# Optimization experiments

Hardware: AMD Instinct MI355X
Metric: run time of the kernel (lower is better)

The kernel has to match this reference:

```python
import jax, jax.numpy as jnp
import numpy as np

B, S, D = 4, 1024, 384
NUM_ITEMS = 16384
NUM_CLUSTERS = 256
MAX_CLUSTER_SIZE = 128  # 16384/256 = 64 real members, padded to 128 with -1
NEG_INF = -1e9


def setup_inputs() -> dict:
    key = jax.random.key(0)
    k1, k2, k3, k4, k5 = jax.random.split(key, 5)
    hidden_states = jax.random.normal(k1, (B, S, D), dtype=jnp.float32)
    item_embeddings = jax.random.normal(k2, (NUM_ITEMS, D), dtype=jnp.float32) * 0.02
    cluster_embeddings = jax.random.normal(k3, (NUM_CLUSTERS, D), dtype=jnp.float32) * 0.02
    targets = jax.random.randint(k4, (B, S), 0, NUM_ITEMS, dtype=jnp.int32)
    item_mask = (jax.random.uniform(k5, (B, S)) < 0.8).astype(jnp.float32)
    # Deterministic round-robin clustering: item i -> cluster i % C, slot i // C
    cluster_assignments = (jnp.arange(NUM_ITEMS, dtype=jnp.int32) % NUM_CLUSTERS)
    ids = (jnp.arange(NUM_CLUSTERS, dtype=jnp.int32)[:, None]
           + NUM_CLUSTERS * jnp.arange(MAX_CLUSTER_SIZE, dtype=jnp.int32)[None, :])
    cluster_indices = jnp.where(ids < NUM_ITEMS, ids, -1)  # [C, M], padded with -1
    in_cluster_id = (jnp.arange(NUM_ITEMS, dtype=jnp.int32) // NUM_CLUSTERS)
    return {
        "hidden_states": hidden_states,
        "item_embeddings": item_embeddings,
        "cluster_embeddings": cluster_embeddings,
        "item_mask": item_mask,
        "targets": targets,
        "cluster_assignments": cluster_assignments,
        "cluster_indices": cluster_indices,
        "in_cluster_id": in_cluster_id,
    }


def reference(hidden_states, item_embeddings, cluster_embeddings, item_mask,
              targets, cluster_assignments, cluster_indices, in_cluster_id):
    # Level 1: cluster logits / log-probs
    cluster_logits = jnp.einsum('bsd,cd->bsc', hidden_states, cluster_embeddings)
    cluster_log_probs = jax.nn.log_softmax(cluster_logits, axis=-1)
    target_cluster_ids = cluster_assignments[targets]                      # [B,S]
    target_cluster_log_prob = jnp.take_along_axis(
        cluster_log_probs, target_cluster_ids[..., None].astype(jnp.int32), axis=-1
    ).squeeze(-1)                                                          # [B,S]

    # Level 2: gather member embeddings of the target cluster, masked softmax
    cluster_members = cluster_indices[target_cluster_ids]                  # [B,S,M]
    member_emb = item_embeddings[jnp.maximum(cluster_members, 0)]          # [B,S,M,D]
    member_logits = jnp.einsum('bsd,bsmd->bsm', hidden_states, member_emb)  # [B,S,M]
    masked_logits = jnp.where(cluster_members != -1, member_logits, NEG_INF)
    member_log_probs = jax.nn.log_softmax(masked_logits, axis=-1)
    target_pos = in_cluster_id[targets]                                    # [B,S]
    target_item_log_prob = jnp.take_along_axis(
        member_log_probs, target_pos[..., None].astype(jnp.int32), axis=-1
    ).squeeze(-1)

    # Combined loss
    loss_per_token = -(target_cluster_log_prob + target_item_log_prob)
    total_loss = jnp.sum(loss_per_token * item_mask) / (jnp.sum(item_mask) + 1e-8)

    cluster_preds = jnp.argmax(cluster_logits, axis=-1)
    cluster_acc = jnp.mean((cluster_preds == target_cluster_ids).astype(jnp.float32))

    dummy_logits = jnp.zeros(hidden_states.shape[:2] + (item_embeddings.shape[0],),
                             dtype=hidden_states.dtype)
    return (dummy_logits, total_loss,
            -jnp.mean(target_cluster_log_prob),
            -jnp.mean(target_item_log_prob),
            cluster_acc)
```

## Files before the change

### kernel.cpp

```cpp
#include <hip/hip_runtime.h>
#include <math.h>

#define Ddim 384
#define D4 96
#define NUM_ITEMS 16384
#define NUM_CLUSTERS 256
#define MCS 128
#define NEG_INF_F (-1e9f)
#define NTOK 4096
#define TPB 16
#define NCB (NTOK / TPB)
#define NFB 512

__device__ __forceinline__ float dot4(const float4& a, const float4& b) {
    return a.x * b.x + a.y * b.y + a.z * b.z + a.w * b.w;
}

__global__ __launch_bounds__(512, 2) void hs_fused(
    const float* __restrict__ hidden,
    const float* __restrict__ item_emb,
    const float* __restrict__ cluster_emb,
    const float* __restrict__ item_mask,
    const int*   __restrict__ targets,
    const int*   __restrict__ cluster_assign,
    const int*   __restrict__ cluster_idx,
    const int*   __restrict__ in_cluster_id,
    float* __restrict__ dummy_out,
    float* __restrict__ ws)
{
    const int bid = blockIdx.x;
    const int tid = threadIdx.x;

    if (bid % 3 != 2) {
        const int fid = (bid / 3) * 2 + (bid % 3);
        float4 z; z.x = z.y = z.z = z.w = 0.f;
        float4* o4 = reinterpret_cast<float4*>(dummy_out)
                     + (size_t)fid * 512 + tid;
        #pragma unroll 8
        for (int i = 0; i < 64; ++i)
            o4[(size_t)i * (NFB * 512)] = z;
        return;
    }

    const int cb    = bid / 3;
    const int t0    = cb * TPB;
    const int lane  = tid & 63;
    const int wave  = tid >> 6;
    const int whalf = wave >> 2;
    const int wq    = wave & 3;
    const int q     = lane >> 4;
    const int r     = lane & 15;

    __shared__ float clog[TPB][NUM_CLUSTERS];
    __shared__ float mlog[TPB][64];

    const int tw = t0 + wq * 4;
    const float4* h4 = reinterpret_cast<const float4*>(hidden);
    float4 hf[4][6];
    #pragma unroll
    for (int j = 0; j < 4; ++j)
        #pragma unroll
        for (int i = 0; i < 6; ++i)
            hf[j][i] = h4[(size_t)(tw + j) * D4 + i * 16 + r];

    const float4* ce4 = reinterpret_cast<const float4*>(cluster_emb);
    #pragma unroll 2
    for (int it = 0; it < 32; ++it) {
        const int c = whalf * 128 + it * 4 + q;
        float4 ce[6];
        #pragma unroll
        for (int i = 0; i < 6; ++i) ce[i] = ce4[(size_t)c * D4 + i * 16 + r];
        float a0 = 0.f, a1 = 0.f, a2 = 0.f, a3 = 0.f;
        #pragma unroll
        for (int i = 0; i < 6; ++i) {
            a0 += dot4(ce[i], hf[0][i]);
            a1 += dot4(ce[i], hf[1][i]);
            a2 += dot4(ce[i], hf[2][i]);
            a3 += dot4(ce[i], hf[3][i]);
        }
        const bool hi8 = (r & 8) != 0;
        float u  = hi8 ? a1 : a0;
        float uS = hi8 ? a0 : a1;
        u += __shfl_xor(uS, 8);
        float w  = hi8 ? a3 : a2;
        float wS = hi8 ? a2 : a3;
        w += __shfl_xor(wS, 8);
        const bool hi4 = (r & 4) != 0;
        float zv = hi4 ? w : u;
        float zS = hi4 ? u : w;
        zv += __shfl_xor(zS, 4);
        zv += __shfl_xor(zv, 2);
        zv += __shfl_xor(zv, 1);
        if ((r & 3) == 0) {
            const int m = (r >> 2) & 3;
            const int tokj = (m == 1) ? 2 : (m == 2) ? 1 : m;
            clog[wq * 4 + tokj][c] = zv;
        }
    }
    __syncthreads();

    const int r8 = lane & 7;
    const int g8 = lane >> 3;
    const float4* ie4 = reinterpret_cast<const float4*>(item_emb);

    #pragma unroll
    for (int p = 0; p < 2; ++p) {
        const int t  = wave * 2 + p;
        const int gt = t0 + t;
        const int tgt  = targets[gt];
        const int tc   = cluster_assign[tgt];
        const int tpos = in_cluster_id[tgt];
        const float msk = item_mask[gt];

        const float v0 = clog[t][lane];
        const float v1 = clog[t][lane + 64];
        const float v2 = clog[t][lane + 128];
        const float v3 = clog[t][lane + 192];
        float bv = v0; int bi = lane;
        if (v1 > bv) { bv = v1; bi = lane + 64;  }
        if (v2 > bv) { bv = v2; bi = lane + 128; }
        if (v3 > bv) { bv = v3; bi = lane + 192; }
        #pragma unroll
        for (int m = 32; m > 0; m >>= 1) {
            const float ov = __shfl_xor(bv, m);
            const int   oi = __shfl_xor(bi, m);
            if (ov > bv || (ov == bv && oi < bi)) { bv = ov; bi = oi; }
        }
        float e = expf(v0 - bv) + expf(v1 - bv) + expf(v2 - bv) + expf(v3 - bv);
        #pragma unroll
        for (int m = 32; m > 0; m >>= 1) e += __shfl_xor(e, m);
        const float lse = bv + logf(e);
        const float tlpc = clog[t][tc] - lse;

        float4 hme[12];
        #pragma unroll
        for (int i = 0; i < 12; ++i)
            hme[i] = h4[(size_t)gt * D4 + i * 8 + r8];
        const int* crow = cluster_idx + (size_t)tc * MCS;
        #pragma unroll 2
        for (int it = 0; it < 8; ++it) {
            const int id = crow[it * 8 + g8];
            const float4* ir = ie4 + (size_t)id * D4;
            float pa = 0.f;
            #pragma unroll
            for (int i = 0; i < 12; ++i) pa += dot4(ir[i * 8 + r8], hme[i]);
            pa += __shfl_xor(pa, 1);
            pa += __shfl_xor(pa, 2);
            pa += __shfl_xor(pa, 4);
            if (r8 == 0) mlog[t][it * 8 + g8] = pa;
        }
        const float w0 = mlog[t][lane];
        float mx = w0;
        #pragma unroll
        for (int m = 32; m > 0; m >>= 1) mx = fmaxf(mx, __shfl_xor(mx, m));
        float e2 = expf(w0 - mx);
        #pragma unroll
        for (int m = 32; m > 0; m >>= 1) e2 += __shfl_xor(e2, m);
        const float tlpi = mlog[t][tpos] - (mx + logf(e2));

        if (lane == 0) {
            ws[NTOK + gt]     = msk;
            ws[2 * NTOK + gt] = tlpc;
            ws[3 * NTOK + gt] = tlpi;
            ws[4 * NTOK + gt] = (bi == tc) ? 1.f : 0.f;
        }
    }
}

__global__ __launch_bounds__(1024) void hs_final(
    const float* __restrict__ ws, float* __restrict__ out)
{
    __shared__ double red[5][1024];
    const int tid = threadIdx.x;
    double a0 = 0, a1 = 0, a2 = 0, a3 = 0, a4 = 0;
    for (int i = tid; i < NTOK; i += 1024) {
        const float msk  = ws[NTOK + i];
        const float tlpc = ws[2 * NTOK + i];
        const float tlpi = ws[3 * NTOK + i];
        a0 += (double)(-(tlpc + tlpi) * msk);
        a1 += (double)msk;
        a2 += (double)tlpc;
        a3 += (double)tlpi;
        a4 += (double)ws[4 * NTOK + i];
    }
    red[0][tid] = a0; red[1][tid] = a1; red[2][tid] = a2;
    red[3][tid] = a3; red[4][tid] = a4;
    __syncthreads();
    for (int s2 = 512; s2 > 0; s2 >>= 1) {
        if (tid < s2) {
            red[0][tid] += red[0][tid + s2];
            red[1][tid] += red[1][tid + s2];
            red[2][tid] += red[2][tid + s2];
            red[3][tid] += red[3][tid + s2];
            red[4][tid] += red[4][tid + s2];
        }
        __syncthreads();
    }
    if (tid == 0) {
        out[0] = (float)(red[0][0] / (red[1][0] + 1e-8));
        out[1] = (float)(-red[2][0] / (double)NTOK);
        out[2] = (float)(-red[3][0] / (double)NTOK);
        out[3] = (float)(red[4][0] / (double)NTOK);
    }
}

extern "C" void kernel_launch(void* const* d_in, const int* in_sizes, int n_in,
                              void* d_out, int out_size, void* d_ws, size_t ws_size,
                              hipStream_t stream) {
    const float* hidden         = (const float*)d_in[0];
    const float* item_emb       = (const float*)d_in[1];
    const float* cluster_emb    = (const float*)d_in[2];
    const float* item_mask      = (const float*)d_in[3];
    const int*   targets        = (const int*)d_in[4];
    const int*   cluster_assign = (const int*)d_in[5];
    const int*   cluster_idx    = (const int*)d_in[6];
    const int*   in_cluster_id  = (const int*)d_in[7];

    float* out = (float*)d_out;
    float* ws  = (float*)d_ws;

    const size_t dummy_elems = (size_t)NTOK * NUM_ITEMS;

    hs_fused<<<NFB + NCB, 512, 0, stream>>>(
        hidden, item_emb, cluster_emb, item_mask, targets,
        cluster_assign, cluster_idx, in_cluster_id, out, ws);
    hs_final<<<1, 1024, 0, stream>>>(ws, out + dummy_elems);
}
```

Before: 121.5 us.

## Make each wave own two tokens end-to-end and reuse hidden registers

The cluster-logit phase now gives each wave two tokens and all 256 clusters, instead of four tokens and half the clusters. Each wave therefore computes the cluster logits for the same tokens it later scores against cluster members. The member-logit phase reuses the hidden-state registers already loaded, using a 16-lane layout, so the second load of hidden rows goes away. The trade-off is half the register reuse of each cluster-embedding load, which doubles the cluster-embedding traffic per wave, and a longer shuffle reduction in the member loop.

```diff
diff --git a/kernel.cpp b/kernel.cpp
--- a/kernel.cpp
+++ b/kernel.cpp
@@ -42,71 +42,55 @@
         return;
     }
 
-    const int cb    = bid / 3;
-    const int t0    = cb * TPB;
-    const int lane  = tid & 63;
-    const int wave  = tid >> 6;
-    const int whalf = wave >> 2;
-    const int wq    = wave & 3;
-    const int q     = lane >> 4;
-    const int r     = lane & 15;
+    const int cb   = bid / 3;
+    const int t0   = cb * TPB;
+    const int lane = tid & 63;
+    const int wave = tid >> 6;
+    const int q    = lane >> 4;
+    const int r    = lane & 15;
 
     __shared__ float clog[TPB][NUM_CLUSTERS];
     __shared__ float mlog[TPB][64];
 
-    const int tw = t0 + wq * 4;
+    const int tw = t0 + wave * 2;
     const float4* h4 = reinterpret_cast<const float4*>(hidden);
-    float4 hf[4][6];
+    float4 hf[2][6];
     #pragma unroll
-    for (int j = 0; j < 4; ++j)
+    for (int j = 0; j < 2; ++j)
         #pragma unroll
         for (int i = 0; i < 6; ++i)
             hf[j][i] = h4[(size_t)(tw + j) * D4 + i * 16 + r];
 
     const float4* ce4 = reinterpret_cast<const float4*>(cluster_emb);
     #pragma unroll 2
-    for (int it = 0; it < 32; ++it) {
-        const int c = whalf * 128 + it * 4 + q;
+    for (int it = 0; it < 64; ++it) {
+        const int c = it * 4 + q;
         float4 ce[6];
         #pragma unroll
         for (int i = 0; i < 6; ++i) ce[i] = ce4[(size_t)c * D4 + i * 16 + r];
-        float a0 = 0.f, a1 = 0.f, a2 = 0.f, a3 = 0.f;
+        float a0 = 0.f, a1 = 0.f;
         #pragma unroll
         for (int i = 0; i < 6; ++i) {
             a0 += dot4(ce[i], hf[0][i]);
             a1 += dot4(ce[i], hf[1][i]);
-            a2 += dot4(ce[i], hf[2][i]);
-            a3 += dot4(ce[i], hf[3][i]);
         }
         const bool hi8 = (r & 8) != 0;
         float u  = hi8 ? a1 : a0;
         float uS = hi8 ? a0 : a1;
         u += __shfl_xor(uS, 8);
-        float w  = hi8 ? a3 : a2;
-        float wS = hi8 ? a2 : a3;
-        w += __shfl_xor(wS, 8);
-        const bool hi4 = (r & 4) != 0;
-        float zv = hi4 ? w : u;
-        float zS = hi4 ? u : w;
-        zv += __shfl_xor(zS, 4);
-        zv += __shfl_xor(zv, 2);
-        zv += __shfl_xor(zv, 1);
-        if ((r & 3) == 0) {
-            const int m = (r >> 2) & 3;
-            const int tokj = (m == 1) ? 2 : (m == 2) ? 1 : m;
-            clog[wq * 4 + tokj][c] = zv;
-        }
+        u += __shfl_xor(u, 4);
+        u += __shfl_xor(u, 2);
+        u += __shfl_xor(u, 1);
+        if ((r & 7) == 0)
+            clog[wave * 2 + ((r >> 3) & 1)][c] = u;
     }
     __syncthreads();
 
-    const int r8 = lane & 7;
-    const int g8 = lane >> 3;
     const float4* ie4 = reinterpret_cast<const float4*>(item_emb);
-
     #pragma unroll
     for (int p = 0; p < 2; ++p) {
-        const int t  = wave * 2 + p;
-        const int gt = t0 + t;
+        const int t   = wave * 2 + p;
+        const int gt  = t0 + t;
         const int tgt  = targets[gt];
         const int tc   = cluster_assign[tgt];
         const int tpos = in_cluster_id[tgt];
@@ -132,22 +116,19 @@
         const float lse = bv + logf(e);
         const float tlpc = clog[t][tc] - lse;
 
-        float4 hme[12];
-        #pragma unroll
-        for (int i = 0; i < 12; ++i)
-            hme[i] = h4[(size_t)gt * D4 + i * 8 + r8];
         const int* crow = cluster_idx + (size_t)tc * MCS;
         #pragma unroll 2
-        for (int it = 0; it < 8; ++it) {
-            const int id = crow[it * 8 + g8];
+        for (int it = 0; it < 16; ++it) {
+            const int id = crow[it * 4 + q];
             const float4* ir = ie4 + (size_t)id * D4;
             float pa = 0.f;
             #pragma unroll
-            for (int i = 0; i < 12; ++i) pa += dot4(ir[i * 8 + r8], hme[i]);
+            for (int i = 0; i < 6; ++i) pa += dot4(ir[i * 16 + r], hf[p][i]);
+            pa += __shfl_xor(pa, 8);
+            pa += __shfl_xor(pa, 4);
+            pa += __shfl_xor(pa, 2);
             pa += __shfl_xor(pa, 1);
-            pa += __shfl_xor(pa, 2);
-            pa += __shfl_xor(pa, 4);
-            if (r8 == 0) mlog[t][it * 8 + g8] = pa;
+            if (r == 0) mlog[t][it * 4 + q] = pa;
         }
         const float w0 = mlog[t][lane];
         float mx = w0;
```

New measurement: 131.7 us. +8.4%, slower.
